# Kernel optimization log

Hardware: AMD Instinct MI355X
Metric: run time of the kernel (lower is better)

Reference implementation:

```python
import jax, jax.numpy as jnp
import numpy as np

N = 100000
E = 1600000
FEAT = 128
EMB = 64
HID = 64
OUT = 16


def _glorot(key, shape):
    fan_in, fan_out = shape[1], shape[0]
    lim = (6.0 / (fan_in + fan_out)) ** 0.5
    return jax.random.uniform(key, shape, jnp.float32, -lim, lim)


def setup_inputs() -> dict:
    key = jax.random.key(0)
    ks = jax.random.split(key, 16)
    return {
        "x_feat": jax.random.normal(ks[0], (N, FEAT), jnp.float32),
        "x_emb": jax.random.normal(ks[1], (N, 2, EMB), jnp.float32),
        "edge_index": jax.random.randint(ks[2], (2, E), 0, N, jnp.int32),
        # layer 0: SAGEConv(FEAT -> HID), Linear(EMB -> HID)
        "Wl0": _glorot(ks[3], (HID, FEAT)),
        "bl0": jnp.zeros((HID,), jnp.float32),
        "Wr0": _glorot(ks[4], (HID, FEAT)),
        "We0": _glorot(ks[5], (HID, EMB)),
        "be0": jnp.zeros((HID,), jnp.float32),
        # layer 1 (last): SAGEConv(HID -> OUT), Linear(EMB==HID -> OUT)
        "Wl1": _glorot(ks[6], (OUT, HID)),
        "bl1": jnp.zeros((OUT,), jnp.float32),
        "Wr1": _glorot(ks[7], (OUT, HID)),
        "We1": _glorot(ks[8], (OUT, HID)),
        "be1": jnp.zeros((OUT,), jnp.float32),
    }


def _sage_conv(x, edge_index, Wl, bl, Wr):
    # PyG SAGEConv with mean aggregation:
    #   out = lin_l(mean_{j in N(i)} x_j) + lin_r(x_i)
    src, dst = edge_index[0], edge_index[1]
    msg = x[src]                                   # [E, C] gather
    agg = jax.ops.segment_sum(msg, dst, num_segments=N)       # [N, C]
    deg = jax.ops.segment_sum(jnp.ones((E,), x.dtype), dst, num_segments=N)
    agg = agg / jnp.maximum(deg, 1.0)[:, None]     # mean over neighbors
    return agg @ Wl.T + bl + x @ Wr.T


def reference(x_feat, x_emb, edge_index,
              Wl0, bl0, Wr0, We0, be0,
              Wl1, bl1, Wr1, We1, be1):
    # forward(x=(x_feat, x_emb), edge_index=...) path, eval mode (dropout p=0)
    e = x_emb.mean(axis=1)                         # [N, EMB]
    # layer 0 (all but last): relu(sage + linear(emb))
    h = _sage_conv(x_feat, edge_index, Wl0, bl0, Wr0)
    e = e @ We0.T + be0
    h = jax.nn.relu(h + e)
    # last layer: no relu
    h = _sage_conv(h, edge_index, Wl1, bl1, Wr1)
    e = e @ We1.T + be1
    return h + e
```

## Files before the change

kernel.cpp:

```cpp
#include <hip/hip_runtime.h>
#include <hip/hip_bf16.h>
#include <cstddef>

#define NN 100000
#define EE 1600000
#define NPB 128
#define NB  782
#define ECH 4096
#define NCH 391
#define CAP 6144

typedef __attribute__((ext_vector_type(8))) short bf16x8;
typedef __attribute__((ext_vector_type(4))) float f32x4;

static inline int ceil_div(int a, int b){ return (a + b - 1) / b; }

__device__ inline unsigned short f2bf(float f){
  union { float f; unsigned u; } v; v.f = f;
  unsigned r = (v.u + 0x7fff + ((v.u >> 16) & 1)) >> 16;
  return (unsigned short)r;
}
__device__ inline float bf2f(unsigned short s){
  union { unsigned u; float f; } v; v.u = ((unsigned)s) << 16;
  return v.f;
}

__global__ void prep_we_kernel(const float* __restrict__ We1, const float* __restrict__ We0,
                               const float* __restrict__ be0, const float* __restrict__ be1,
                               float* __restrict__ wee, float* __restrict__ b1e){
  int idx = blockIdx.x * blockDim.x + threadIdx.x;
  if (idx < 16 * 64){
    int i = idx >> 6, j = idx & 63;
    float s = 0.f;
    for (int k = 0; k < 64; k++) s += We1[i * 64 + k] * We0[k * 64 + j];
    wee[idx] = s;
  } else if (idx < 16 * 64 + 16){
    int i = idx - 16 * 64;
    float s = be1[i];
    for (int k = 0; k < 64; k++) s += We1[i * 64 + k] * be0[k];
    b1e[i] = s;
  }
}

__global__ void prep_wcat_kernel(const float* __restrict__ Wl0, const float* __restrict__ Wr0,
                                 const float* __restrict__ We0, const float* __restrict__ wee,
                                 unsigned short* __restrict__ wcat){
  int idx = blockIdx.x * blockDim.x + threadIdx.x;
  if (idx >= 144 * 192) return;
  int n = idx / 192, k = idx % 192;
  float v;
  if (n < 64)       v = (k < 128) ? Wl0[n * 128 + k] : 0.f;
  else if (n < 128) v = (k < 128) ? Wr0[(n - 64) * 128 + k] : We0[(n - 64) * 64 + (k - 128)];
  else              v = (k < 128) ? 0.f : wee[(n - 128) * 64 + (k - 128)];
  wcat[idx] = f2bf(v);
}

__global__ __launch_bounds__(256) void ehist_kernel(const int* __restrict__ dst,
                                                    int* __restrict__ ghist){
  __shared__ int lh[NB];
  for (int i = threadIdx.x; i < NB; i += 256) lh[i] = 0;
  __syncthreads();
  for (int i = blockIdx.x * blockDim.x + threadIdx.x; i < EE; i += gridDim.x * blockDim.x)
    atomicAdd(&lh[dst[i] >> 7], 1);
  __syncthreads();
  for (int i = threadIdx.x; i < NB; i += 256){
    int c = lh[i];
    if (c) atomicAdd(&ghist[i], c);
  }
}

__global__ void escan_kernel(const int* __restrict__ ghist, int* __restrict__ boff,
                             int* __restrict__ cur){
  __shared__ int s[1024];
  int t = threadIdx.x;
  int v = (t < NB) ? ghist[t] : 0;
  s[t] = v;
  __syncthreads();
  for (int off = 1; off < 1024; off <<= 1){
    int x = (t >= off) ? s[t - off] : 0;
    __syncthreads();
    s[t] += x;
    __syncthreads();
  }
  if (t < NB){ int e = s[t] - v; boff[t] = e; cur[t] = e; }
  if (t == 0) boff[NB] = EE;
}

__global__ __launch_bounds__(256) void escatter_kernel(const int* __restrict__ src,
                                                       const int* __restrict__ dst,
                                                       int* __restrict__ cur,
                                                       int* __restrict__ ebkt){
  __shared__ int ls[ECH];
  __shared__ int ld[ECH];
  __shared__ int lh[NB];
  __shared__ int lo[NB];
  int t = threadIdx.x;
  int e0 = blockIdx.x * ECH;
  int ne = EE - e0; if (ne > ECH) ne = ECH;
  for (int i = t; i < NB; i += 256) lh[i] = 0;
  __syncthreads();
  for (int i = t; i < ne; i += 256){
    int d = dst[e0 + i];
    ls[i] = src[e0 + i];
    ld[i] = d;
    atomicAdd(&lh[d >> 7], 1);
  }
  __syncthreads();
  for (int i = t; i < NB; i += 256){
    int c = lh[i];
    lo[i] = c ? atomicAdd(&cur[i], c) : 0;
    lh[i] = 0;
  }
  __syncthreads();
  for (int i = t; i < ne; i += 256){
    int d = ld[i], b = d >> 7;
    int r = atomicAdd(&lh[b], 1);
    ebkt[lo[b] + r] = ((d & 127) << 24) | ls[i];
  }
}

__global__ __launch_bounds__(256) void bsort_kernel(
    const int* __restrict__ boff, const int* __restrict__ ebkt,
    int* __restrict__ ssrc, int* __restrict__ rs, int* __restrict__ deg){
  __shared__ int lraw[CAP];
  __shared__ int lout[CAP];
  __shared__ int lh[NPB];
  __shared__ int loff[NPB];
  __shared__ int lcur[NPB];
  const int t = threadIdx.x;
  const int b = blockIdx.x;
  const int e0 = boff[b];
  int cnt = boff[b + 1] - e0;
  if (cnt > CAP) cnt = CAP;
  for (int i = t; i < NPB; i += 256) lh[i] = 0;
  __syncthreads();
  for (int i = t; i < cnt; i += 256){
    int w = ebkt[e0 + i];
    lraw[i] = w;
    atomicAdd(&lh[((unsigned)w) >> 24], 1);
  }
  __syncthreads();
  {
    int v = (t < NPB) ? lh[t] : 0;
    int s = v;
    for (int off = 1; off < NPB; off <<= 1){
      int x = 0;
      if (t < NPB && t >= off) x = loff[t - off];
      __syncthreads();
      if (t < NPB) loff[t] = s;
      __syncthreads();
      if (t < NPB && t >= off) s += loff[t - off];
      __syncthreads();
    }
    if (t < NPB){ loff[t] = s - v; lcur[t] = s - v; }
  }
  __syncthreads();
  for (int i = t; i < cnt; i += 256){
    int w = lraw[i];
    int d = ((unsigned)w) >> 24;
    int pos = atomicAdd(&lcur[d], 1);
    lout[pos] = w & 0xFFFFFF;
  }
  __syncthreads();
  for (int i = t; i < cnt; i += 256) ssrc[e0 + i] = lout[i];
  if (t < NPB){
    int node = b * NPB + t;
    if (node < NN){
      rs[node] = e0 + loff[t];
      deg[node] = lh[t];
    }
  }
}

__global__ __launch_bounds__(256) void l0_gemm_kernel(
    const float* __restrict__ x_feat, const float* __restrict__ x_emb,
    const unsigned short* __restrict__ wcat,
    unsigned short* __restrict__ y0, float* __restrict__ re0, float* __restrict__ eo, int M){
  __shared__ unsigned short As[64 * 200];
  const int t = threadIdx.x;
  const int row0 = blockIdx.x * 64;
  for (int idx = t; idx < 64 * 48; idx += 256){
    int r = idx / 48, q = idx % 48;
    int row = row0 + r;
    float4 v = make_float4(0.f, 0.f, 0.f, 0.f);
    if (row < M){
      if (q < 32){
        v = ((const float4*)x_feat)[(size_t)row * 32 + q];
      } else {
        float4 a = ((const float4*)x_emb)[(size_t)row * 32 + (q - 32)];
        float4 b = ((const float4*)x_emb)[(size_t)row * 32 + 16 + (q - 32)];
        v.x = 0.5f * (a.x + b.x); v.y = 0.5f * (a.y + b.y);
        v.z = 0.5f * (a.z + b.z); v.w = 0.5f * (a.w + b.w);
      }
    }
    ushort4 u; u.x = f2bf(v.x); u.y = f2bf(v.y); u.z = f2bf(v.z); u.w = f2bf(v.w);
    *(ushort4*)&As[r * 200 + q * 4] = u;
  }
  const int w = t >> 6, l = t & 63;
  const int lm = l & 15, quad = l >> 4;
  bf16x8 bfr0[6], bfr1[6], bfr2[6];
  {
    int n0 = (w * 2 + 0) * 16 + lm;
    int n1 = (w * 2 + 1) * 16 + lm;
    #pragma unroll
    for (int ks = 0; ks < 6; ks++){
      bfr0[ks] = *(const bf16x8*)&wcat[n0 * 192 + ks * 32 + quad * 8];
      bfr1[ks] = *(const bf16x8*)&wcat[n1 * 192 + ks * 32 + quad * 8];
    }
    if (w == 3){
      int n2 = 128 + lm;
      #pragma unroll
      for (int ks = 0; ks < 6; ks++)
        bfr2[ks] = *(const bf16x8*)&wcat[n2 * 192 + ks * 32 + quad * 8];
    }
  }
  __syncthreads();
  for (int rg = 0; rg < 4; rg++){
    bf16x8 af[6];
    #pragma unroll
    for (int ks = 0; ks < 6; ks++)
      af[ks] = *(const bf16x8*)&As[(rg * 16 + lm) * 200 + ks * 32 + quad * 8];
    f32x4 acc0 = {0.f, 0.f, 0.f, 0.f};
    f32x4 acc1 = {0.f, 0.f, 0.f, 0.f};
    f32x4 acc2 = {0.f, 0.f, 0.f, 0.f};
    #pragma unroll
    for (int ks = 0; ks < 6; ks++){
      acc0 = __builtin_amdgcn_mfma_f32_16x16x32_bf16(af[ks], bfr0[ks], acc0, 0, 0, 0);
      acc1 = __builtin_amdgcn_mfma_f32_16x16x32_bf16(af[ks], bfr1[ks], acc1, 0, 0, 0);
    }
    if (w == 3){
      #pragma unroll
      for (int ks = 0; ks < 6; ks++)
        acc2 = __builtin_amdgcn_mfma_f32_16x16x32_bf16(af[ks], bfr2[ks], acc2, 0, 0, 0);
    }
    #pragma unroll
    for (int r = 0; r < 4; r++){
      int grow = row0 + rg * 16 + quad * 4 + r;
      if (grow < M){
        if (w < 2){
          y0[(size_t)grow * 64 + w * 32 + lm]      = f2bf(acc0[r]);
          y0[(size_t)grow * 64 + w * 32 + 16 + lm] = f2bf(acc1[r]);
        } else {
          re0[(size_t)grow * 64 + (w - 2) * 32 + lm]      = acc0[r];
          re0[(size_t)grow * 64 + (w - 2) * 32 + 16 + lm] = acc1[r];
          if (w == 3) eo[(size_t)grow * 16 + lm] = acc2[r];
        }
      }
    }
  }
}

__global__ void agg0_kernel(const unsigned short* __restrict__ y0,
                            const float4* __restrict__ re0,
                            const float* __restrict__ bl0, const float* __restrict__ be0,
                            const int* __restrict__ rs, const int* __restrict__ deg,
                            const int* __restrict__ ssrc, float4* __restrict__ h){
  int g = blockIdx.x * blockDim.x + threadIdx.x;
  if (g >= NN * 16) return;
  int node = g >> 4, lane = g & 15;
  int start = rs[node], cnt = deg[node];
  float acc[4][4] = {};
  int i = 0;
  for (; i + 4 <= cnt; i += 4){
    int s0 = ssrc[start + i + 0], s1 = ssrc[start + i + 1];
    int s2 = ssrc[start + i + 2], s3 = ssrc[start + i + 3];
    ushort4 v0 = *(const ushort4*)&y0[(size_t)s0 * 64 + lane * 4];
    ushort4 v1 = *(const ushort4*)&y0[(size_t)s1 * 64 + lane * 4];
    ushort4 v2 = *(const ushort4*)&y0[(size_t)s2 * 64 + lane * 4];
    ushort4 v3 = *(const ushort4*)&y0[(size_t)s3 * 64 + lane * 4];
    acc[0][0] += bf2f(v0.x); acc[0][1] += bf2f(v0.y); acc[0][2] += bf2f(v0.z); acc[0][3] += bf2f(v0.w);
    acc[1][0] += bf2f(v1.x); acc[1][1] += bf2f(v1.y); acc[1][2] += bf2f(v1.z); acc[1][3] += bf2f(v1.w);
    acc[2][0] += bf2f(v2.x); acc[2][1] += bf2f(v2.y); acc[2][2] += bf2f(v2.z); acc[2][3] += bf2f(v2.w);
    acc[3][0] += bf2f(v3.x); acc[3][1] += bf2f(v3.y); acc[3][2] += bf2f(v3.z); acc[3][3] += bf2f(v3.w);
  }
  for (; i < cnt; i++){
    int s = ssrc[start + i];
    ushort4 v = *(const ushort4*)&y0[(size_t)s * 64 + lane * 4];
    acc[0][0] += bf2f(v.x); acc[0][1] += bf2f(v.y); acc[0][2] += bf2f(v.z); acc[0][3] += bf2f(v.w);
  }
  float sx = (acc[0][0] + acc[1][0]) + (acc[2][0] + acc[3][0]);
  float sy = (acc[0][1] + acc[1][1]) + (acc[2][1] + acc[3][1]);
  float sz = (acc[0][2] + acc[1][2]) + (acc[2][2] + acc[3][2]);
  float sw = (acc[0][3] + acc[1][3]) + (acc[2][3] + acc[3][3]);
  float inv = 1.0f / (float)(cnt > 1 ? cnt : 1);
  float4 rr = re0[(size_t)node * 16 + lane];
  float4 b1 = ((const float4*)bl0)[lane];
  float4 b2 = ((const float4*)be0)[lane];
  float4 v;
  v.x = sx * inv + rr.x + b1.x + b2.x;
  v.y = sy * inv + rr.y + b1.y + b2.y;
  v.z = sz * inv + rr.z + b1.z + b2.z;
  v.w = sw * inv + rr.w + b1.w + b2.w;
  v.x = v.x > 0.f ? v.x : 0.f;
  v.y = v.y > 0.f ? v.y : 0.f;
  v.z = v.z > 0.f ? v.z : 0.f;
  v.w = v.w > 0.f ? v.w : 0.f;
  h[(size_t)node * 16 + lane] = v;
}

__global__ __launch_bounds__(256) void gemm16_dual_kernel(
    const float* __restrict__ H, const float* __restrict__ eo,
    const float* __restrict__ Wl1, const float* __restrict__ Wr1,
    const float* __restrict__ bl1, const float* __restrict__ b1e,
    unsigned short* __restrict__ Y1, float* __restrict__ Out, int M){
  __shared__ float Hs[64][65];
  __shared__ float Wls[16][65];
  __shared__ float Wrs[16][65];
  __shared__ float bs[16];
  const int t = threadIdx.x;
  const int row0 = blockIdx.x * 64;
  {
    int j = t >> 4, kq = t & 15;
    float4 a = ((const float4*)Wl1)[j * 16 + kq];
    float4 b = ((const float4*)Wr1)[j * 16 + kq];
    Wls[j][kq*4+0]=a.x; Wls[j][kq*4+1]=a.y; Wls[j][kq*4+2]=a.z; Wls[j][kq*4+3]=a.w;
    Wrs[j][kq*4+0]=b.x; Wrs[j][kq*4+1]=b.y; Wrs[j][kq*4+2]=b.z; Wrs[j][kq*4+3]=b.w;
  }
  if (t < 16) bs[t] = bl1[t] + b1e[t];
  for (int idx = t; idx < 64 * 16; idx += 256){
    int n = idx >> 4, kq = idx & 15;
    int row = row0 + n;
    float4 v = make_float4(0.f,0.f,0.f,0.f);
    if (row < M) v = ((const float4*)H)[(size_t)row * 16 + kq];
    Hs[n][kq*4+0]=v.x; Hs[n][kq*4+1]=v.y; Hs[n][kq*4+2]=v.z; Hs[n][kq*4+3]=v.w;
  }
  __syncthreads();
  const int n = t >> 2, jq = t & 3;
  float y[4] = {}, o[4] = {};
  #pragma unroll 4
  for (int k = 0; k < 64; k++){
    float a = Hs[n][k];
    #pragma unroll
    for (int j = 0; j < 4; j++){
      y[j] = fmaf(a, Wls[jq*4 + j][k], y[j]);
      o[j] = fmaf(a, Wrs[jq*4 + j][k], o[j]);
    }
  }
  int row = row0 + n;
  if (row < M){
    ushort4 yb; yb.x = f2bf(y[0]); yb.y = f2bf(y[1]); yb.z = f2bf(y[2]); yb.w = f2bf(y[3]);
    *(ushort4*)&Y1[(size_t)row * 16 + jq * 4] = yb;
    float4 ev = ((const float4*)eo)[(size_t)row * 4 + jq];
    ((float4*)Out)[(size_t)row * 4 + jq] =
        make_float4(o[0] + ev.x + bs[jq*4+0], o[1] + ev.y + bs[jq*4+1],
                    o[2] + ev.z + bs[jq*4+2], o[3] + ev.w + bs[jq*4+3]);
  }
}

__global__ void agg1_kernel(const unsigned short* __restrict__ y1,
                            const int* __restrict__ rs, const int* __restrict__ deg,
                            const int* __restrict__ ssrc, float4* __restrict__ outp){
  int g = blockIdx.x * blockDim.x + threadIdx.x;
  if (g >= NN * 4) return;
  int node = g >> 2, lane = g & 3;
  int start = rs[node], cnt = deg[node];
  float acc[4][4] = {};
  int i = 0;
  for (; i + 4 <= cnt; i += 4){
    int s0 = ssrc[start + i + 0], s1 = ssrc[start + i + 1];
    int s2 = ssrc[start + i + 2], s3 = ssrc[start + i + 3];
    ushort4 v0 = *(const ushort4*)&y1[(size_t)s0 * 16 + lane * 4];
    ushort4 v1 = *(const ushort4*)&y1[(size_t)s1 * 16 + lane * 4];
    ushort4 v2 = *(const ushort4*)&y1[(size_t)s2 * 16 + lane * 4];
    ushort4 v3 = *(const ushort4*)&y1[(size_t)s3 * 16 + lane * 4];
    acc[0][0] += bf2f(v0.x); acc[0][1] += bf2f(v0.y); acc[0][2] += bf2f(v0.z); acc[0][3] += bf2f(v0.w);
    acc[1][0] += bf2f(v1.x); acc[1][1] += bf2f(v1.y); acc[1][2] += bf2f(v1.z); acc[1][3] += bf2f(v1.w);
    acc[2][0] += bf2f(v2.x); acc[2][1] += bf2f(v2.y); acc[2][2] += bf2f(v2.z); acc[2][3] += bf2f(v2.w);
    acc[3][0] += bf2f(v3.x); acc[3][1] += bf2f(v3.y); acc[3][2] += bf2f(v3.z); acc[3][3] += bf2f(v3.w);
  }
  for (; i < cnt; i++){
    int s = ssrc[start + i];
    ushort4 v = *(const ushort4*)&y1[(size_t)s * 16 + lane * 4];
    acc[0][0] += bf2f(v.x); acc[0][1] += bf2f(v.y); acc[0][2] += bf2f(v.z); acc[0][3] += bf2f(v.w);
  }
  float sx = (acc[0][0] + acc[1][0]) + (acc[2][0] + acc[3][0]);
  float sy = (acc[0][1] + acc[1][1]) + (acc[2][1] + acc[3][1]);
  float sz = (acc[0][2] + acc[1][2]) + (acc[2][2] + acc[3][2]);
  float sw = (acc[0][3] + acc[1][3]) + (acc[2][3] + acc[3][3]);
  float inv = 1.0f / (float)(cnt > 1 ? cnt : 1);
  float4 o = outp[(size_t)node * 4 + lane];
  o.x += sx * inv;
  o.y += sy * inv;
  o.z += sz * inv;
  o.w += sw * inv;
  outp[(size_t)node * 4 + lane] = o;
}

extern "C" void kernel_launch(void* const* d_in, const int* in_sizes, int n_in,
                              void* d_out, int out_size, void* d_ws, size_t ws_size,
                              hipStream_t stream){
  (void)in_sizes; (void)n_in; (void)out_size; (void)ws_size;
  const float* x_feat = (const float*)d_in[0];
  const float* x_emb  = (const float*)d_in[1];
  const int*   ei     = (const int*)d_in[2];
  const float* Wl0 = (const float*)d_in[3];
  const float* bl0 = (const float*)d_in[4];
  const float* Wr0 = (const float*)d_in[5];
  const float* We0 = (const float*)d_in[6];
  const float* be0 = (const float*)d_in[7];
  const float* Wl1 = (const float*)d_in[8];
  const float* bl1 = (const float*)d_in[9];
  const float* Wr1 = (const float*)d_in[10];
  const float* We1 = (const float*)d_in[11];
  const float* be1 = (const float*)d_in[12];
  float* out = (float*)d_out;

  char* w = (char*)d_ws;
  float* re0   = (float*)w;                 w += sizeof(float) * (size_t)NN * 64;
  float* h     = (float*)w;                 w += sizeof(float) * (size_t)NN * 64;
  float* eo    = (float*)w;                 w += sizeof(float) * (size_t)NN * 16;
  unsigned short* y0 = (unsigned short*)w;  w += sizeof(unsigned short) * (size_t)NN * 64;
  unsigned short* y1 = (unsigned short*)w;  w += sizeof(unsigned short) * (size_t)NN * 16;
  unsigned short* wcat = (unsigned short*)w; w += sizeof(unsigned short) * 144 * 192;
  float* wee   = (float*)w;                 w += sizeof(float) * 16 * 64;
  float* b1e   = (float*)w;                 w += sizeof(float) * 16;
  int* ebkt    = (int*)w;                   w += sizeof(int) * (size_t)EE;
  int* ssrc    = (int*)w;                   w += sizeof(int) * (size_t)EE;
  int* ghist   = (int*)w;                   w += sizeof(int) * NB;
  int* boff    = (int*)w;                   w += sizeof(int) * (NB + 1);
  int* cur     = (int*)w;                   w += sizeof(int) * NB;
  int* rs      = (int*)w;                   w += sizeof(int) * NN;
  int* deg     = (int*)w;                   w += sizeof(int) * NN;

  const int* srcp = ei;
  const int* dstp = ei + EE;

  hipMemsetAsync(ghist, 0, sizeof(int) * NB, stream);

  prep_we_kernel<<<5, 256, 0, stream>>>(We1, We0, be0, be1, wee, b1e);
  prep_wcat_kernel<<<ceil_div(144 * 192, 256), 256, 0, stream>>>(Wl0, Wr0, We0, wee, wcat);

  ehist_kernel<<<512, 256, 0, stream>>>(dstp, ghist);
  escan_kernel<<<1, 1024, 0, stream>>>(ghist, boff, cur);
  escatter_kernel<<<NCH, 256, 0, stream>>>(srcp, dstp, cur, ebkt);
  bsort_kernel<<<NB, 256, 0, stream>>>(boff, ebkt, ssrc, rs, deg);

  l0_gemm_kernel<<<ceil_div(NN, 64), 256, 0, stream>>>(x_feat, x_emb, wcat, y0, re0, eo, NN);

  agg0_kernel<<<ceil_div(NN * 16, 256), 256, 0, stream>>>(
      y0, (const float4*)re0, bl0, be0, rs, deg, ssrc, (float4*)h);

  gemm16_dual_kernel<<<ceil_div(NN, 64), 256, 0, stream>>>(h, eo, Wl1, Wr1, bl1, b1e,
                                                           y1, out, NN);
  agg1_kernel<<<ceil_div(NN * 4, 256), 256, 0, stream>>>(y1, rs, deg, ssrc, (float4*)out);
}
```

Before: 331.9 us.

## Drop histogram/scan pass with fixed-capacity buckets; restructure layer-0 GEMM and gathers

Removes the edge histogram and scan kernels. Edges are scattered into fixed-capacity per-bucket slots (CAP each), and the sort is done in place, so the separate ssrc array goes away. The layer-0 GEMM drops the extra wee tile and instead writes a bf16 copy of the mean embedding. The emb-to-output term is folded into gemm16_dual via wee. The GEMM also batches its global loads before the conversion, gains a launch_bounds occupancy hint, and the gather loops are unrolled to 8 outstanding loads. Edges beyond a bucket's capacity are silently dropped, so the change relies on the degree distribution staying under CAP.

```diff
diff --git a/kernel.cpp b/kernel.cpp
--- a/kernel.cpp
+++ b/kernel.cpp
@@ -43,55 +43,21 @@
 }
 
 __global__ void prep_wcat_kernel(const float* __restrict__ Wl0, const float* __restrict__ Wr0,
-                                 const float* __restrict__ We0, const float* __restrict__ wee,
+                                 const float* __restrict__ We0,
                                  unsigned short* __restrict__ wcat){
   int idx = blockIdx.x * blockDim.x + threadIdx.x;
-  if (idx >= 144 * 192) return;
+  if (idx >= 128 * 192) return;
   int n = idx / 192, k = idx % 192;
   float v;
-  if (n < 64)       v = (k < 128) ? Wl0[n * 128 + k] : 0.f;
-  else if (n < 128) v = (k < 128) ? Wr0[(n - 64) * 128 + k] : We0[(n - 64) * 64 + (k - 128)];
-  else              v = (k < 128) ? 0.f : wee[(n - 128) * 64 + (k - 128)];
+  if (n < 64) v = (k < 128) ? Wl0[n * 128 + k] : 0.f;
+  else        v = (k < 128) ? Wr0[(n - 64) * 128 + k] : We0[(n - 64) * 64 + (k - 128)];
   wcat[idx] = f2bf(v);
-}
-
-__global__ __launch_bounds__(256) void ehist_kernel(const int* __restrict__ dst,
-                                                    int* __restrict__ ghist){
-  __shared__ int lh[NB];
-  for (int i = threadIdx.x; i < NB; i += 256) lh[i] = 0;
-  __syncthreads();
-  for (int i = blockIdx.x * blockDim.x + threadIdx.x; i < EE; i += gridDim.x * blockDim.x)
-    atomicAdd(&lh[dst[i] >> 7], 1);
-  __syncthreads();
-  for (int i = threadIdx.x; i < NB; i += 256){
-    int c = lh[i];
-    if (c) atomicAdd(&ghist[i], c);
-  }
-}
-
-__global__ void escan_kernel(const int* __restrict__ ghist, int* __restrict__ boff,
-                             int* __restrict__ cur){
-  __shared__ int s[1024];
-  int t = threadIdx.x;
-  int v = (t < NB) ? ghist[t] : 0;
-  s[t] = v;
-  __syncthreads();
-  for (int off = 1; off < 1024; off <<= 1){
-    int x = (t >= off) ? s[t - off] : 0;
-    __syncthreads();
-    s[t] += x;
-    __syncthreads();
-  }
-  if (t < NB){ int e = s[t] - v; boff[t] = e; cur[t] = e; }
-  if (t == 0) boff[NB] = EE;
 }
 
 __global__ __launch_bounds__(256) void escatter_kernel(const int* __restrict__ src,
                                                        const int* __restrict__ dst,
                                                        int* __restrict__ cur,
                                                        int* __restrict__ ebkt){
-  __shared__ int ls[ECH];
-  __shared__ int ld[ECH];
   __shared__ int lh[NB];
   __shared__ int lo[NB];
   int t = threadIdx.x;
@@ -99,12 +65,8 @@
   int ne = EE - e0; if (ne > ECH) ne = ECH;
   for (int i = t; i < NB; i += 256) lh[i] = 0;
   __syncthreads();
-  for (int i = t; i < ne; i += 256){
-    int d = dst[e0 + i];
-    ls[i] = src[e0 + i];
-    ld[i] = d;
-    atomicAdd(&lh[d >> 7], 1);
-  }
+  for (int i = t; i < ne; i += 256)
+    atomicAdd(&lh[dst[e0 + i] >> 7], 1);
   __syncthreads();
   for (int i = t; i < NB; i += 256){
     int c = lh[i];
@@ -113,15 +75,16 @@
   }
   __syncthreads();
   for (int i = t; i < ne; i += 256){
-    int d = ld[i], b = d >> 7;
+    int d = dst[e0 + i], b = d >> 7;
     int r = atomicAdd(&lh[b], 1);
-    ebkt[lo[b] + r] = ((d & 127) << 24) | ls[i];
+    int p = lo[b] + r;
+    if (p < CAP) ebkt[b * CAP + p] = ((d & 127) << 24) | src[e0 + i];
   }
 }
 
 __global__ __launch_bounds__(256) void bsort_kernel(
-    const int* __restrict__ boff, const int* __restrict__ ebkt,
-    int* __restrict__ ssrc, int* __restrict__ rs, int* __restrict__ deg){
+    const int* __restrict__ cur, int* __restrict__ ebkt,
+    int* __restrict__ rs, int* __restrict__ deg){
   __shared__ int lraw[CAP];
   __shared__ int lout[CAP];
   __shared__ int lh[NPB];
@@ -129,8 +92,8 @@
   __shared__ int lcur[NPB];
   const int t = threadIdx.x;
   const int b = blockIdx.x;
-  const int e0 = boff[b];
-  int cnt = boff[b + 1] - e0;
+  const int e0 = b * CAP;
+  int cnt = cur[b];
   if (cnt > CAP) cnt = CAP;
   for (int i = t; i < NPB; i += 256) lh[i] = 0;
   __syncthreads();
@@ -162,56 +125,69 @@
     lout[pos] = w & 0xFFFFFF;
   }
   __syncthreads();
-  for (int i = t; i < cnt; i += 256) ssrc[e0 + i] = lout[i];
+  for (int i = t; i < cnt; i += 256) ebkt[e0 + i] = lout[i];
   if (t < NPB){
     int node = b * NPB + t;
     if (node < NN){
-      rs[node] = e0 + loff[t];
+      rs[node]  = e0 + loff[t];
       deg[node] = lh[t];
     }
   }
 }
 
-__global__ __launch_bounds__(256) void l0_gemm_kernel(
+__global__ __launch_bounds__(256, 4) void l0_gemm_kernel(
     const float* __restrict__ x_feat, const float* __restrict__ x_emb,
     const unsigned short* __restrict__ wcat,
-    unsigned short* __restrict__ y0, float* __restrict__ re0, float* __restrict__ eo, int M){
+    unsigned short* __restrict__ y0, float* __restrict__ re0,
+    unsigned short* __restrict__ e_bf, int M){
   __shared__ unsigned short As[64 * 200];
   const int t = threadIdx.x;
   const int row0 = blockIdx.x * 64;
-  for (int idx = t; idx < 64 * 48; idx += 256){
+  float4 tmpa[12], tmpb[12];
+  int rr[12], qq[12];
+  #pragma unroll
+  for (int k = 0; k < 12; k++){
+    int idx = t + k * 256;
     int r = idx / 48, q = idx % 48;
+    rr[k] = r; qq[k] = q;
     int row = row0 + r;
     float4 v = make_float4(0.f, 0.f, 0.f, 0.f);
+    float4 u = make_float4(0.f, 0.f, 0.f, 0.f);
     if (row < M){
       if (q < 32){
         v = ((const float4*)x_feat)[(size_t)row * 32 + q];
       } else {
-        float4 a = ((const float4*)x_emb)[(size_t)row * 32 + (q - 32)];
-        float4 b = ((const float4*)x_emb)[(size_t)row * 32 + 16 + (q - 32)];
-        v.x = 0.5f * (a.x + b.x); v.y = 0.5f * (a.y + b.y);
-        v.z = 0.5f * (a.z + b.z); v.w = 0.5f * (a.w + b.w);
+        v = ((const float4*)x_emb)[(size_t)row * 32 + (q - 32)];
+        u = ((const float4*)x_emb)[(size_t)row * 32 + 16 + (q - 32)];
       }
     }
-    ushort4 u; u.x = f2bf(v.x); u.y = f2bf(v.y); u.z = f2bf(v.z); u.w = f2bf(v.w);
-    *(ushort4*)&As[r * 200 + q * 4] = u;
+    tmpa[k] = v; tmpb[k] = u;
+  }
+  #pragma unroll
+  for (int k = 0; k < 12; k++){
+    int r = rr[k], q = qq[k];
+    int row = row0 + r;
+    float4 v = tmpa[k];
+    if (q >= 32){
+      float4 u = tmpb[k];
+      v.x = 0.5f * (v.x + u.x); v.y = 0.5f * (v.y + u.y);
+      v.z = 0.5f * (v.z + u.z); v.w = 0.5f * (v.w + u.w);
+    }
+    ushort4 s; s.x = f2bf(v.x); s.y = f2bf(v.y); s.z = f2bf(v.z); s.w = f2bf(v.w);
+    *(ushort4*)&As[r * 200 + q * 4] = s;
+    if (q >= 32 && row < M)
+      *(ushort4*)&e_bf[(size_t)row * 64 + (q - 32) * 4] = s;
   }
   const int w = t >> 6, l = t & 63;
   const int lm = l & 15, quad = l >> 4;
-  bf16x8 bfr0[6], bfr1[6], bfr2[6];
+  bf16x8 bfr0[6], bfr1[6];
   {
-    int n0 = (w * 2 + 0) * 16 + lm;
-    int n1 = (w * 2 + 1) * 16 + lm;
+    int n0 = w * 16 + lm;
+    int n1 = 64 + w * 16 + lm;
     #pragma unroll
     for (int ks = 0; ks < 6; ks++){
       bfr0[ks] = *(const bf16x8*)&wcat[n0 * 192 + ks * 32 + quad * 8];
       bfr1[ks] = *(const bf16x8*)&wcat[n1 * 192 + ks * 32 + quad * 8];
-    }
-    if (w == 3){
-      int n2 = 128 + lm;
-      #pragma unroll
-      for (int ks = 0; ks < 6; ks++)
-        bfr2[ks] = *(const bf16x8*)&wcat[n2 * 192 + ks * 32 + quad * 8];
     }
   }
   __syncthreads();
@@ -222,29 +198,17 @@
       af[ks] = *(const bf16x8*)&As[(rg * 16 + lm) * 200 + ks * 32 + quad * 8];
     f32x4 acc0 = {0.f, 0.f, 0.f, 0.f};
     f32x4 acc1 = {0.f, 0.f, 0.f, 0.f};
-    f32x4 acc2 = {0.f, 0.f, 0.f, 0.f};
     #pragma unroll
     for (int ks = 0; ks < 6; ks++){
       acc0 = __builtin_amdgcn_mfma_f32_16x16x32_bf16(af[ks], bfr0[ks], acc0, 0, 0, 0);
       acc1 = __builtin_amdgcn_mfma_f32_16x16x32_bf16(af[ks], bfr1[ks], acc1, 0, 0, 0);
     }
-    if (w == 3){
-      #pragma unroll
-      for (int ks = 0; ks < 6; ks++)
-        acc2 = __builtin_amdgcn_mfma_f32_16x16x32_bf16(af[ks], bfr2[ks], acc2, 0, 0, 0);
-    }
     #pragma unroll
     for (int r = 0; r < 4; r++){
       int grow = row0 + rg * 16 + quad * 4 + r;
       if (grow < M){
-        if (w < 2){
-          y0[(size_t)grow * 64 + w * 32 + lm]      = f2bf(acc0[r]);
-          y0[(size_t)grow * 64 + w * 32 + 16 + lm] = f2bf(acc1[r]);
-        } else {
-          re0[(size_t)grow * 64 + (w - 2) * 32 + lm]      = acc0[r];
-          re0[(size_t)grow * 64 + (w - 2) * 32 + 16 + lm] = acc1[r];
-          if (w == 3) eo[(size_t)grow * 16 + lm] = acc2[r];
-        }
+        y0[(size_t)grow * 64 + w * 16 + lm]  = f2bf(acc0[r]);
+        re0[(size_t)grow * 64 + w * 16 + lm] = acc1[r];
       }
     }
   }
@@ -261,17 +225,29 @@
   int start = rs[node], cnt = deg[node];
   float acc[4][4] = {};
   int i = 0;
+  for (; i + 8 <= cnt; i += 8){
+    int s[8];
+    #pragma unroll
+    for (int j = 0; j < 8; j++) s[j] = ssrc[start + i + j];
+    ushort4 v[8];
+    #pragma unroll
+    for (int j = 0; j < 8; j++) v[j] = *(const ushort4*)&y0[(size_t)s[j] * 64 + lane * 4];
+    #pragma unroll
+    for (int j = 0; j < 8; j++){
+      acc[j & 3][0] += bf2f(v[j].x); acc[j & 3][1] += bf2f(v[j].y);
+      acc[j & 3][2] += bf2f(v[j].z); acc[j & 3][3] += bf2f(v[j].w);
+    }
+  }
   for (; i + 4 <= cnt; i += 4){
-    int s0 = ssrc[start + i + 0], s1 = ssrc[start + i + 1];
-    int s2 = ssrc[start + i + 2], s3 = ssrc[start + i + 3];
-    ushort4 v0 = *(const ushort4*)&y0[(size_t)s0 * 64 + lane * 4];
-    ushort4 v1 = *(const ushort4*)&y0[(size_t)s1 * 64 + lane * 4];
-    ushort4 v2 = *(const ushort4*)&y0[(size_t)s2 * 64 + lane * 4];
-    ushort4 v3 = *(const ushort4*)&y0[(size_t)s3 * 64 + lane * 4];
-    acc[0][0] += bf2f(v0.x); acc[0][1] += bf2f(v0.y); acc[0][2] += bf2f(v0.z); acc[0][3] += bf2f(v0.w);
-    acc[1][0] += bf2f(v1.x); acc[1][1] += bf2f(v1.y); acc[1][2] += bf2f(v1.z); acc[1][3] += bf2f(v1.w);
-    acc[2][0] += bf2f(v2.x); acc[2][1] += bf2f(v2.y); acc[2][2] += bf2f(v2.z); acc[2][3] += bf2f(v2.w);
-    acc[3][0] += bf2f(v3.x); acc[3][1] += bf2f(v3.y); acc[3][2] += bf2f(v3.z); acc[3][3] += bf2f(v3.w);
+    int s[4];
+    #pragma unroll
+    for (int j = 0; j < 4; j++) s[j] = ssrc[start + i + j];
+    #pragma unroll
+    for (int j = 0; j < 4; j++){
+      ushort4 v = *(const ushort4*)&y0[(size_t)s[j] * 64 + lane * 4];
+      acc[j][0] += bf2f(v.x); acc[j][1] += bf2f(v.y);
+      acc[j][2] += bf2f(v.z); acc[j][3] += bf2f(v.w);
+    }
   }
   for (; i < cnt; i++){
     int s = ssrc[start + i];
@@ -283,14 +259,14 @@
   float sz = (acc[0][2] + acc[1][2]) + (acc[2][2] + acc[3][2]);
   float sw = (acc[0][3] + acc[1][3]) + (acc[2][3] + acc[3][3]);
   float inv = 1.0f / (float)(cnt > 1 ? cnt : 1);
-  float4 rr = re0[(size_t)node * 16 + lane];
+  float4 rv = re0[(size_t)node * 16 + lane];
   float4 b1 = ((const float4*)bl0)[lane];
   float4 b2 = ((const float4*)be0)[lane];
   float4 v;
-  v.x = sx * inv + rr.x + b1.x + b2.x;
-  v.y = sy * inv + rr.y + b1.y + b2.y;
-  v.z = sz * inv + rr.z + b1.z + b2.z;
-  v.w = sw * inv + rr.w + b1.w + b2.w;
+  v.x = sx * inv + rv.x + b1.x + b2.x;
+  v.y = sy * inv + rv.y + b1.y + b2.y;
+  v.z = sz * inv + rv.z + b1.z + b2.z;
+  v.w = sw * inv + rv.w + b1.w + b2.w;
   v.x = v.x > 0.f ? v.x : 0.f;
   v.y = v.y > 0.f ? v.y : 0.f;
   v.z = v.z > 0.f ? v.z : 0.f;
@@ -299,13 +275,16 @@
 }
 
 __global__ __launch_bounds__(256) void gemm16_dual_kernel(
-    const float* __restrict__ H, const float* __restrict__ eo,
+    const float* __restrict__ H, const unsigned short* __restrict__ E,
     const float* __restrict__ Wl1, const float* __restrict__ Wr1,
+    const float* __restrict__ wee,
     const float* __restrict__ bl1, const float* __restrict__ b1e,
     unsigned short* __restrict__ Y1, float* __restrict__ Out, int M){
   __shared__ float Hs[64][65];
+  __shared__ float Es[64][65];
   __shared__ float Wls[16][65];
   __shared__ float Wrs[16][65];
+  __shared__ float Wes[16][65];
   __shared__ float bs[16];
   const int t = threadIdx.x;
   const int row0 = blockIdx.x * 64;
@@ -313,16 +292,23 @@
     int j = t >> 4, kq = t & 15;
     float4 a = ((const float4*)Wl1)[j * 16 + kq];
     float4 b = ((const float4*)Wr1)[j * 16 + kq];
+    float4 c = ((const float4*)wee)[j * 16 + kq];
     Wls[j][kq*4+0]=a.x; Wls[j][kq*4+1]=a.y; Wls[j][kq*4+2]=a.z; Wls[j][kq*4+3]=a.w;
     Wrs[j][kq*4+0]=b.x; Wrs[j][kq*4+1]=b.y; Wrs[j][kq*4+2]=b.z; Wrs[j][kq*4+3]=b.w;
+    Wes[j][kq*4+0]=c.x; Wes[j][kq*4+1]=c.y; Wes[j][kq*4+2]=c.z; Wes[j][kq*4+3]=c.w;
   }
   if (t < 16) bs[t] = bl1[t] + b1e[t];
   for (int idx = t; idx < 64 * 16; idx += 256){
     int n = idx >> 4, kq = idx & 15;
     int row = row0 + n;
     float4 v = make_float4(0.f,0.f,0.f,0.f);
-    if (row < M) v = ((const float4*)H)[(size_t)row * 16 + kq];
+    ushort4 u = make_ushort4(0, 0, 0, 0);
+    if (row < M){
+      v = ((const float4*)H)[(size_t)row * 16 + kq];
+      u = *(const ushort4*)&E[(size_t)row * 64 + kq * 4];
+    }
     Hs[n][kq*4+0]=v.x; Hs[n][kq*4+1]=v.y; Hs[n][kq*4+2]=v.z; Hs[n][kq*4+3]=v.w;
+    Es[n][kq*4+0]=bf2f(u.x); Es[n][kq*4+1]=bf2f(u.y); Es[n][kq*4+2]=bf2f(u.z); Es[n][kq*4+3]=bf2f(u.w);
   }
   __syncthreads();
   const int n = t >> 2, jq = t & 3;
@@ -330,20 +316,20 @@
   #pragma unroll 4
   for (int k = 0; k < 64; k++){
     float a = Hs[n][k];
+    float e = Es[n][k];
     #pragma unroll
     for (int j = 0; j < 4; j++){
       y[j] = fmaf(a, Wls[jq*4 + j][k], y[j]);
       o[j] = fmaf(a, Wrs[jq*4 + j][k], o[j]);
+      o[j] = fmaf(e, Wes[jq*4 + j][k], o[j]);
     }
   }
   int row = row0 + n;
   if (row < M){
     ushort4 yb; yb.x = f2bf(y[0]); yb.y = f2bf(y[1]); yb.z = f2bf(y[2]); yb.w = f2bf(y[3]);
     *(ushort4*)&Y1[(size_t)row * 16 + jq * 4] = yb;
-    float4 ev = ((const float4*)eo)[(size_t)row * 4 + jq];
     ((float4*)Out)[(size_t)row * 4 + jq] =
-        make_float4(o[0] + ev.x + bs[jq*4+0], o[1] + ev.y + bs[jq*4+1],
-                    o[2] + ev.z + bs[jq*4+2], o[3] + ev.w + bs[jq*4+3]);
+        make_float4(o[0] + bs[jq*4+0], o[1] + bs[jq*4+1], o[2] + bs[jq*4+2], o[3] + bs[jq*4+3]);
   }
 }
 
@@ -356,17 +342,29 @@
   int start = rs[node], cnt = deg[node];
   float acc[4][4] = {};
   int i = 0;
+  for (; i + 8 <= cnt; i += 8){
+    int s[8];
+    #pragma unroll
+    for (int j = 0; j < 8; j++) s[j] = ssrc[start + i + j];
+    ushort4 v[8];
+    #pragma unroll
+    for (int j = 0; j < 8; j++) v[j] = *(const ushort4*)&y1[(size_t)s[j] * 16 + lane * 4];
+    #pragma unroll
+    for (int j = 0; j < 8; j++){
+      acc[j & 3][0] += bf2f(v[j].x); acc[j & 3][1] += bf2f(v[j].y);
+      acc[j & 3][2] += bf2f(v[j].z); acc[j & 3][3] += bf2f(v[j].w);
+    }
+  }
   for (; i + 4 <= cnt; i += 4){
-    int s0 = ssrc[start + i + 0], s1 = ssrc[start + i + 1];
-    int s2 = ssrc[start + i + 2], s3 = ssrc[start + i + 3];
-    ushort4 v0 = *(const ushort4*)&y1[(size_t)s0 * 16 + lane * 4];
-    ushort4 v1 = *(const ushort4*)&y1[(size_t)s1 * 16 + lane * 4];
-    ushort4 v2 = *(const ushort4*)&y1[(size_t)s2 * 16 + lane * 4];
-    ushort4 v3 = *(const ushort4*)&y1[(size_t)s3 * 16 + lane * 4];
-    acc[0][0] += bf2f(v0.x); acc[0][1] += bf2f(v0.y); acc[0][2] += bf2f(v0.z); acc[0][3] += bf2f(v0.w);
-    acc[1][0] += bf2f(v1.x); acc[1][1] += bf2f(v1.y); acc[1][2] += bf2f(v1.z); acc[1][3] += bf2f(v1.w);
-    acc[2][0] += bf2f(v2.x); acc[2][1] += bf2f(v2.y); acc[2][2] += bf2f(v2.z); acc[2][3] += bf2f(v2.w);
-    acc[3][0] += bf2f(v3.x); acc[3][1] += bf2f(v3.y); acc[3][2] += bf2f(v3.z); acc[3][3] += bf2f(v3.w);
+    int s[4];
+    #pragma unroll
+    for (int j = 0; j < 4; j++) s[j] = ssrc[start + i + j];
+    #pragma unroll
+    for (int j = 0; j < 4; j++){
+      ushort4 v = *(const ushort4*)&y1[(size_t)s[j] * 16 + lane * 4];
+      acc[j][0] += bf2f(v.x); acc[j][1] += bf2f(v.y);
+      acc[j][2] += bf2f(v.z); acc[j][3] += bf2f(v.w);
+    }
   }
   for (; i < cnt; i++){
     int s = ssrc[start + i];
@@ -406,41 +404,36 @@
   float* out = (float*)d_out;
 
   char* w = (char*)d_ws;
-  float* re0   = (float*)w;                 w += sizeof(float) * (size_t)NN * 64;
-  float* h     = (float*)w;                 w += sizeof(float) * (size_t)NN * 64;
-  float* eo    = (float*)w;                 w += sizeof(float) * (size_t)NN * 16;
-  unsigned short* y0 = (unsigned short*)w;  w += sizeof(unsigned short) * (size_t)NN * 64;
-  unsigned short* y1 = (unsigned short*)w;  w += sizeof(unsigned short) * (size_t)NN * 16;
-  unsigned short* wcat = (unsigned short*)w; w += sizeof(unsigned short) * 144 * 192;
-  float* wee   = (float*)w;                 w += sizeof(float) * 16 * 64;
-  float* b1e   = (float*)w;                 w += sizeof(float) * 16;
-  int* ebkt    = (int*)w;                   w += sizeof(int) * (size_t)EE;
-  int* ssrc    = (int*)w;                   w += sizeof(int) * (size_t)EE;
-  int* ghist   = (int*)w;                   w += sizeof(int) * NB;
-  int* boff    = (int*)w;                   w += sizeof(int) * (NB + 1);
-  int* cur     = (int*)w;                   w += sizeof(int) * NB;
-  int* rs      = (int*)w;                   w += sizeof(int) * NN;
-  int* deg     = (int*)w;                   w += sizeof(int) * NN;
+  float* re0   = (float*)w;                  w += sizeof(float) * (size_t)NN * 64;
+  float* h     = (float*)w;                  w += sizeof(float) * (size_t)NN * 64;
+  unsigned short* y0  = (unsigned short*)w;  w += sizeof(unsigned short) * (size_t)NN * 64;
+  unsigned short* e_bf= (unsigned short*)w;  w += sizeof(unsigned short) * (size_t)NN * 64;
+  unsigned short* y1  = (unsigned short*)w;  w += sizeof(unsigned short) * (size_t)NN * 16;
+  unsigned short* wcat= (unsigned short*)w;  w += sizeof(unsigned short) * 128 * 192;
+  float* wee   = (float*)w;                  w += sizeof(float) * 16 * 64;
+  float* b1e   = (float*)w;                  w += sizeof(float) * 16;
+  int* ebkt    = (int*)w;                    w += sizeof(int) * (size_t)NB * CAP;
+  int* cur     = (int*)w;                    w += sizeof(int) * NB;
+  int* rs      = (int*)w;                    w += sizeof(int) * NN;
+  int* deg     = (int*)w;                    w += sizeof(int) * NN;
 
   const int* srcp = ei;
   const int* dstp = ei + EE;
 
-  hipMemsetAsync(ghist, 0, sizeof(int) * NB, stream);
+  hipMemsetAsync(cur, 0, sizeof(int) * NB, stream);
 
   prep_we_kernel<<<5, 256, 0, stream>>>(We1, We0, be0, be1, wee, b1e);
-  prep_wcat_kernel<<<ceil_div(144 * 192, 256), 256, 0, stream>>>(Wl0, Wr0, We0, wee, wcat);
-
-  ehist_kernel<<<512, 256, 0, stream>>>(dstp, ghist);
-  escan_kernel<<<1, 1024, 0, stream>>>(ghist, boff, cur);
+  prep_wcat_kernel<<<ceil_div(128 * 192, 256), 256, 0, stream>>>(Wl0, Wr0, We0, wcat);
+
   escatter_kernel<<<NCH, 256, 0, stream>>>(srcp, dstp, cur, ebkt);
-  bsort_kernel<<<NB, 256, 0, stream>>>(boff, ebkt, ssrc, rs, deg);
-
-  l0_gemm_kernel<<<ceil_div(NN, 64), 256, 0, stream>>>(x_feat, x_emb, wcat, y0, re0, eo, NN);
+  bsort_kernel<<<NB, 256, 0, stream>>>(cur, ebkt, rs, deg);
+
+  l0_gemm_kernel<<<ceil_div(NN, 64), 256, 0, stream>>>(x_feat, x_emb, wcat, y0, re0, e_bf, NN);
 
   agg0_kernel<<<ceil_div(NN * 16, 256), 256, 0, stream>>>(
-      y0, (const float4*)re0, bl0, be0, rs, deg, ssrc, (float4*)h);
-
-  gemm16_dual_kernel<<<ceil_div(NN, 64), 256, 0, stream>>>(h, eo, Wl1, Wr1, bl1, b1e,
-                                                           y1, out, NN);
-  agg1_kernel<<<ceil_div(NN * 4, 256), 256, 0, stream>>>(y1, rs, deg, ssrc, (float4*)out);
-}
+      y0, (const float4*)re0, bl0, be0, rs, deg, ebkt, (float4*)h);
+
+  gemm16_dual_kernel<<<ceil_div(NN, 64), 256, 0, stream>>>(h, e_bf, Wl1, Wr1, wee,
+                                                           bl1, b1e, y1, out, NN);
+  agg1_kernel<<<ceil_div(NN * 4, 256), 256, 0, stream>>>(y1, rs, deg, ebkt, (float4*)out);
+}
```

Result: no change. 336.0 us (+1.2%).
